# Performance work log

Measured on AMD Instinct MI355X. Metric: run time of the kernel, lower is better.

## Reference

```python
import jax, jax.numpy as jnp
import numpy as np

EPS = 1.1920929e-07  # torch RMSNorm default eps = finfo(float32).eps


def segsum(a):
    # a: (..., T) -> (..., T, T); [i, j] = sum_{j < t <= i} a[t] for j <= i, -inf above diag
    T = a.shape[-1]
    cs = jnp.cumsum(a, axis=-1)
    diff = cs[..., :, None] - cs[..., None, :]
    mask = jnp.tril(jnp.ones((T, T), dtype=bool))
    return jnp.where(mask, diff, -jnp.inf)


def dw_causal_conv(x, w):
    # x: (B, L, C), w: (C, K) depthwise causal conv (left pad K-1), matches Conv1d(pad=K-1)[:, :L]
    K = w.shape[-1]
    L = x.shape[1]
    xp = jnp.pad(x, ((0, 0), (K - 1, 0), (0, 0)))
    out = jnp.zeros_like(x)
    for j in range(K):
        out = out + xp[:, j:j + L, :] * w[:, j]
    return out


def ssd(X, A, Bv, Cv, block_len, init_state):
    # X: (B,L,H,P) pre-multiplied by dt; A: (B,L,H) = A*dt; Bv/Cv: (B,L,H,N)
    Bsz, L, H, P = X.shape
    N = Bv.shape[-1]
    c = L // block_len
    Xb = X.reshape(Bsz, c, block_len, H, P)
    Bb = Bv.reshape(Bsz, c, block_len, H, N)
    Cb = Cv.reshape(Bsz, c, block_len, H, N)
    Ab = A.reshape(Bsz, c, block_len, H).transpose(0, 3, 1, 2)  # (B,H,c,l)
    A_cumsum = jnp.cumsum(Ab, axis=-1)
    Ltri = jnp.exp(segsum(Ab))  # (B,H,c,l,l)
    # intra-chunk (diagonal block) output
    Y_diag = jnp.einsum('bclhn,bcshn,bhcls,bcshp->bclhp', Cb, Bb, Ltri, Xb)
    # per-chunk final states
    decay_states = jnp.exp(A_cumsum[..., -1:] - A_cumsum)  # (B,H,c,l)
    states = jnp.einsum('bclhn,bhcl,bclhp->bchpn', Bb, decay_states, Xb)
    states = jnp.concatenate([init_state[:, None], states], axis=1)  # (B,c+1,H,P,N)
    # inter-chunk recurrence via segsum over chunk boundaries
    last_A = A_cumsum[..., -1]  # (B,H,c)
    decay_chunk = jnp.exp(segsum(jnp.pad(last_A, ((0, 0), (0, 0), (1, 0)))))  # (B,H,c+1,c+1)
    new_states = jnp.einsum('bhzc,bchpn->bzhpn', decay_chunk, states)
    states, final_state = new_states[:, :-1], new_states[:, -1]
    # off-diagonal contribution from carried-in states
    state_decay_out = jnp.exp(A_cumsum)  # (B,H,c,l)
    Y_off = jnp.einsum('bclhn,bchpn,bhcl->bclhp', Cb, states, state_decay_out)
    Y = (Y_diag + Y_off).reshape(Bsz, L, H, P)
    return Y, final_state


def setup_inputs():
    key = jax.random.key(0)
    ks = jax.random.split(key, 8)
    d_model, d_state, d_conv, expand, headdim, ngroups = 1024, 128, 4, 2, 64, 1
    d_inner = expand * d_model                      # 2048
    H = d_inner // headdim                          # 32
    proj_out = 2 * d_inner + 2 * ngroups * d_state + H  # 4384
    conv_dim = d_inner + 2 * ngroups * d_state      # 2304
    B, L = 2, 2048
    x = jax.random.normal(ks[0], (B, L, d_model), dtype=jnp.float32)
    state = jnp.zeros((B, H, headdim, d_state), dtype=jnp.float32)
    in_proj_w = jax.random.normal(ks[1], (proj_out, d_model), dtype=jnp.float32) * 0.02
    conv_w = jax.random.normal(ks[2], (conv_dim, d_conv), dtype=jnp.float32) * 0.2
    A_log = jnp.log(jax.random.uniform(ks[3], (H,), minval=1.0, maxval=16.0))
    dt0 = jnp.exp(jax.random.uniform(ks[4], (H,)) * (np.log(0.1) - np.log(0.001)) + np.log(0.001))
    dt0 = jnp.maximum(dt0, 0.0001)
    dt_bias = dt0 + jnp.log(-jnp.expm1(-dt0))
    D_param = jnp.ones((H,), dtype=jnp.float32)
    norm_w = jnp.ones((d_inner,), dtype=jnp.float32)
    out_proj_w = jax.random.normal(ks[5], (d_model, d_inner), dtype=jnp.float32) * 0.02
    return dict(x=x, state=state, in_proj_w=in_proj_w, conv_w=conv_w, A_log=A_log,
                dt_bias=dt_bias, D_param=D_param, norm_w=norm_w, out_proj_w=out_proj_w,
                block_len=64)


def reference(x, state, in_proj_w, conv_w, A_log, dt_bias, D_param, norm_w, out_proj_w, block_len):
    B, L, Dm = x.shape
    H = A_log.shape[0]
    P = state.shape[2]
    N = state.shape[3]
    d_inner = H * P
    conv_dim = conv_w.shape[0]
    zxbcdt = x @ in_proj_w.T  # (B,L,proj_out)
    z = zxbcdt[..., :d_inner]
    xBC = zxbcdt[..., d_inner:d_inner + conv_dim]
    dt = zxbcdt[..., d_inner + conv_dim:]
    xBC = jax.nn.silu(dw_causal_conv(xBC, conv_w))
    x_branch = xBC[..., :d_inner]
    Bv = xBC[..., d_inner:d_inner + N]           # ngroups = 1
    Cv = xBC[..., d_inner + N:]
    X = jax.nn.silu(x_branch.reshape(B, L, H, P))
    Bv = jnp.broadcast_to(jax.nn.silu(Bv)[:, :, None, :], (B, L, H, N))
    Cv = jnp.broadcast_to(jax.nn.silu(Cv)[:, :, None, :], (B, L, H, N))
    A = -jnp.exp(A_log)
    dt = jax.nn.softplus(dt + dt_bias)           # (B,L,H)
    A_dt = A * dt
    X_dt = X * dt[..., None]
    Y, final_state = ssd(X_dt, A_dt, Bv, Cv, block_len, state)
    Y = Y + D_param[None, None, :, None] * X
    y_flat = Y.reshape(B, L, d_inner)
    y_norm = y_flat * jax.lax.rsqrt(jnp.mean(y_flat * y_flat, axis=-1, keepdims=True) + EPS) * norm_w
    y_core = y_norm * jax.nn.sigmoid(z)
    y = y_core @ out_proj_w.T + x
    return (y, final_state)
```

## Files before the change

kernel.cpp:

```cpp
#include <hip/hip_runtime.h>
#include <math.h>

#define BATCH 2
#define LSEQ  2048
#define TTOK  4096
#define DM    1024
#define DI    2048
#define NH    32
#define HP    64
#define NS    128
#define CONVD 2304
#define PROJ  4384
#define NCH   32
#define BLK   64

typedef __bf16 bf16x8 __attribute__((ext_vector_type(8)));
typedef float  f32x4  __attribute__((ext_vector_type(4)));
typedef unsigned short ushortx8 __attribute__((ext_vector_type(8)));
typedef unsigned short ushort_t;
typedef __attribute__((address_space(3))) void  lds_void;
typedef __attribute__((address_space(1))) const void glb_cvoid;

__device__ __forceinline__ float silu_(float x) { return x / (1.f + __expf(-x)); }

__device__ __forceinline__ unsigned short f2bf(float x) {
    union { float f; unsigned u; } u; u.f = x;
    unsigned r = u.u + 0x7fffu + ((u.u >> 16) & 1u);
    return (unsigned short)(r >> 16);
}
__device__ __forceinline__ float bf2f(unsigned short s) {
    union { unsigned u; float f; } u; u.u = ((unsigned)s) << 16; return u.f;
}

__global__ __launch_bounds__(256)
void cast_all_k(const float* __restrict__ x, const float* __restrict__ ipw,
                const float* __restrict__ opw,
                ushort_t* __restrict__ xb, ushort_t* __restrict__ ipb,
                ushort_t* __restrict__ opb)
{
    const int n1 = TTOK*DM, n2 = PROJ*DM;
    int i = (blockIdx.x * 256 + threadIdx.x) * 8;
    const float* src; ushort_t* dst;
    if (i < n1)            { src = x   + i;             dst = xb  + i; }
    else if (i < n1 + n2)  { src = ipw + (i - n1);      dst = ipb + (i - n1); }
    else                   { src = opw + (i - n1 - n2); dst = opb + (i - n1 - n2); }
    float4 a = *(const float4*)(src);
    float4 b = *(const float4*)(src + 4);
    ushortx8 r;
    r[0]=f2bf(a.x); r[1]=f2bf(a.y); r[2]=f2bf(a.z); r[3]=f2bf(a.w);
    r[4]=f2bf(b.x); r[5]=f2bf(b.y); r[6]=f2bf(b.z); r[7]=f2bf(b.w);
    *(ushortx8*)dst = r;
}

template<int HASRES, int OUTBF>
__global__ __launch_bounds__(256)
void hgemm_nt(const ushort_t* __restrict__ A, const ushort_t* __restrict__ Bw,
              void* __restrict__ Cp, const float* __restrict__ R,
              int M, int N, int K)
{
    __shared__ ushort_t As[128 * 32];
    __shared__ ushort_t Bs[128 * 32];
    const int t = threadIdx.x;
    const int l = t & 63, w = t >> 6;
    const int tx_ = (N + 127) >> 7, ty_ = (M + 127) >> 7;
    int bid = blockIdx.x;
    int sc = bid / (8 * ty_), rem = bid % (8 * ty_);
    int sw_w = min(8, tx_ - sc * 8);
    int bx = sc * 8 + rem % sw_w;
    int by = rem / sw_w;
    const int bm = by * 128, bn = bx * 128;
    const int wm = (w >> 1) * 64, wn = (w & 1) * 64;

    const int srow = t >> 2;
    const int skk  = (t & 3) * 8;
    const ushort_t* Ag0 = A + (size_t)(bm + srow)      * K + skk;
    const ushort_t* Ag1 = A + (size_t)(bm + 64 + srow) * K + skk;
    const int bn0 = min(bn + srow, N - 1), bn1 = min(bn + 64 + srow, N - 1);
    const ushort_t* Bg0 = Bw + (size_t)bn0 * K + skk;
    const ushort_t* Bg1 = Bw + (size_t)bn1 * K + skk;
    char* As0 = (char*)As;
    char* Bs0 = (char*)Bs;
    const int la0 = 16 * t;
    const int la1 = 4096 + 16 * t;

    f32x4 acc[4][4] = {};
    const int fr = l & 15, koff = (l >> 4) * 8;

    for (int k0 = 0; k0 < K; k0 += 32) {
        __syncthreads();
        __builtin_amdgcn_global_load_lds((glb_cvoid*)(Ag0 + k0), (lds_void*)(As0 + la0), 16, 0, 0);
        __builtin_amdgcn_global_load_lds((glb_cvoid*)(Ag1 + k0), (lds_void*)(As0 + la1), 16, 0, 0);
        __builtin_amdgcn_global_load_lds((glb_cvoid*)(Bg0 + k0), (lds_void*)(Bs0 + la0), 16, 0, 0);
        __builtin_amdgcn_global_load_lds((glb_cvoid*)(Bg1 + k0), (lds_void*)(Bs0 + la1), 16, 0, 0);
        __syncthreads();
        bf16x8 af[4], bfr[4];
#pragma unroll
        for (int mt = 0; mt < 4; ++mt)
            af[mt] = *(const bf16x8*)(As + (wm + mt * 16 + fr) * 32 + koff);
#pragma unroll
        for (int nt = 0; nt < 4; ++nt)
            bfr[nt] = *(const bf16x8*)(Bs + (wn + nt * 16 + fr) * 32 + koff);
#pragma unroll
        for (int mt = 0; mt < 4; ++mt)
#pragma unroll
            for (int nt = 0; nt < 4; ++nt)
                acc[mt][nt] = __builtin_amdgcn_mfma_f32_16x16x32_bf16(af[mt], bfr[nt], acc[mt][nt], 0, 0, 0);
    }

    const int crow = (l >> 4) * 4, ccol = l & 15;
#pragma unroll
    for (int mt = 0; mt < 4; ++mt) {
#pragma unroll
        for (int nt = 0; nt < 4; ++nt) {
            int n = bn + wn + nt * 16 + ccol;
            if (n >= N) continue;
#pragma unroll
            for (int i = 0; i < 4; ++i) {
                int m = bm + wm + mt * 16 + crow + i;
                float v = acc[mt][nt][i];
                if (HASRES) v += R[(size_t)m * N + n];
                if (OUTBF) ((ushort_t*)Cp)[(size_t)m * N + n] = f2bf(v);
                else       ((float*)Cp)[(size_t)m * N + n] = v;
            }
        }
    }
}

#define NCONVB 9216
__global__ __launch_bounds__(256)
void mid1_k(const ushort_t* __restrict__ zx, const float* __restrict__ cw,
            const float* __restrict__ dt_bias, const float* __restrict__ A_log,
            ushort_t* __restrict__ xBC, float* __restrict__ dt_sp, float* __restrict__ cumA)
{
    if (blockIdx.x < NCONVB) {
        int idx = blockIdx.x * 256 + threadIdx.x;
        int c4 = (idx % (CONVD/4)) * 4;
        int tkk = idx / (CONVD/4);
        int b = tkk >> 11, l = tkk & 2047;
        const ushort_t* col = zx + (size_t)b * LSEQ * PROJ + DI + c4;
        float4 w0 = *(const float4*)(cw + c4*4);
        float4 w1 = *(const float4*)(cw + c4*4 + 4);
        float4 w2 = *(const float4*)(cw + c4*4 + 8);
        float4 w3 = *(const float4*)(cw + c4*4 + 12);
        ushort4 tp = *(const ushort4*)(col + (size_t)l * PROJ);
        float a0 = w0.w * bf2f(tp.x), a1 = w1.w * bf2f(tp.y), a2 = w2.w * bf2f(tp.z), a3 = w3.w * bf2f(tp.w);
        if (l >= 1) { ushort4 v = *(const ushort4*)(col + (size_t)(l-1) * PROJ);
            a0 += w0.z*bf2f(v.x); a1 += w1.z*bf2f(v.y); a2 += w2.z*bf2f(v.z); a3 += w3.z*bf2f(v.w); }
        if (l >= 2) { ushort4 v = *(const ushort4*)(col + (size_t)(l-2) * PROJ);
            a0 += w0.y*bf2f(v.x); a1 += w1.y*bf2f(v.y); a2 += w2.y*bf2f(v.z); a3 += w3.y*bf2f(v.w); }
        if (l >= 3) { ushort4 v = *(const ushort4*)(col + (size_t)(l-3) * PROJ);
            a0 += w0.x*bf2f(v.x); a1 += w1.x*bf2f(v.y); a2 += w2.x*bf2f(v.z); a3 += w3.x*bf2f(v.w); }
        ushort4 o;
        o.x = f2bf(silu_(silu_(a0))); o.y = f2bf(silu_(silu_(a1)));
        o.z = f2bf(silu_(silu_(a2))); o.w = f2bf(silu_(silu_(a3)));
        *(ushort4*)(xBC + (size_t)tkk * CONVD + c4) = o;
    } else {
        int wid = (blockIdx.x - NCONVB) * 4 + (threadIdx.x >> 6);
        int ln = threadIdx.x & 63;
        int c = wid & 31, h = (wid >> 5) & 31, b = wid >> 10;
        int tk = b * LSEQ + c * BLK + ln;
        float xv = bf2f(zx[(size_t)tk * PROJ + (DI + CONVD) + h]) + dt_bias[h];
        float dtv = (xv > 20.f) ? xv : log1pf(__expf(xv));
        dt_sp[tk * NH + h] = dtv;
        float val = -__expf(A_log[h]) * dtv;
#pragma unroll
        for (int off = 1; off < 64; off <<= 1) {
            float u = __shfl_up(val, off, 64);
            if (ln >= off) val += u;
        }
        cumA[(size_t)wid * 64 + ln] = val;
    }
}

__global__ __launch_bounds__(256)
void mid2_k(const ushort_t* __restrict__ xBC, const float* __restrict__ dt_sp,
            const float* __restrict__ cumA, float* __restrict__ CBT,
            float* __restrict__ states)
{
    __shared__ __align__(16) char smem[33408];
    int t = threadIdx.x, r = t >> 2, q = t & 3;
    if (blockIdx.x < 64) {
        int b = blockIdx.x >> 5, c = blockIdx.x & 31;
        float (*sB)[65] = (float(*)[65])smem;
        float (*sC)[65] = sB + 64;
        const ushort_t* xb = xBC + (size_t)(b * LSEQ + c * BLK) * CONVD;
        float acc[16];
#pragma unroll
        for (int i = 0; i < 16; ++i) acc[i] = 0.f;
        for (int half = 0; half < 2; ++half) {
            __syncthreads();
#pragma unroll
            for (int jj = 0; jj < 4; ++jj) {
                ushort4 bv = *(const ushort4*)(xb + (size_t)r * CONVD + DI      + half*64 + q*16 + jj*4);
                ushort4 cv = *(const ushort4*)(xb + (size_t)r * CONVD + DI + NS + half*64 + q*16 + jj*4);
                int col = q*16 + jj*4;
                sB[r][col]=bf2f(bv.x); sB[r][col+1]=bf2f(bv.y); sB[r][col+2]=bf2f(bv.z); sB[r][col+3]=bf2f(bv.w);
                sC[r][col]=bf2f(cv.x); sC[r][col+1]=bf2f(cv.y); sC[r][col+2]=bf2f(cv.z); sC[r][col+3]=bf2f(cv.w);
            }
            __syncthreads();
            for (int n = 0; n < 64; ++n) {
                float cv = sC[r][n];
#pragma unroll
                for (int si = 0; si < 16; ++si)
                    acc[si] += cv * sB[q*16 + si][n];
            }
        }
        float* o = CBT + (size_t)blockIdx.x * 4096 + r * 64 + q * 16;
#pragma unroll
        for (int si = 0; si < 16; ++si) o[si] = acc[si];
    } else {
        int bi = blockIdx.x - 64;
        int h = bi & 31, c = (bi >> 5) & 31, b = bi >> 10;
        ushort_t* XdT = (ushort_t*)smem;
        ushort_t* BdT = XdT + 64 * 72;
        const float* cA = cumA + (size_t)((b*NH + h)*NCH + c) * 64;
        float scale = dt_sp[(b * LSEQ + c * BLK + r) * NH + h] * __expf(cA[63] - cA[r]);
        const ushort_t* xb = xBC + (size_t)(b * LSEQ + c * BLK + r) * CONVD;
#pragma unroll
        for (int jj = 0; jj < 4; ++jj) {
            ushort4 v = *(const ushort4*)(xb + h*HP + q*16 + jj*4);
            int p0 = q*16 + jj*4;
            XdT[(p0+0)*72 + r] = v.x; XdT[(p0+1)*72 + r] = v.y;
            XdT[(p0+2)*72 + r] = v.z; XdT[(p0+3)*72 + r] = v.w;
        }
#pragma unroll
        for (int jj = 0; jj < 8; ++jj) {
            ushort4 v = *(const ushort4*)(xb + DI + q*32 + jj*4);
            int n0 = q*32 + jj*4;
            BdT[(n0+0)*72 + r] = f2bf(bf2f(v.x)*scale);
            BdT[(n0+1)*72 + r] = f2bf(bf2f(v.y)*scale);
            BdT[(n0+2)*72 + r] = f2bf(bf2f(v.z)*scale);
            BdT[(n0+3)*72 + r] = f2bf(bf2f(v.w)*scale);
        }
        __syncthreads();
        int ln = t & 63, w = t >> 6;
        int wm = (w >> 1) * 32, wn = (w & 1) * 64;
        int fr = ln & 15;
        f32x4 acc[2][4] = {};
#pragma unroll
        for (int ks = 0; ks < 2; ++ks) {
            int koff = ks*32 + (ln >> 4) * 8;
            bf16x8 af[2], bv[4];
#pragma unroll
            for (int mt = 0; mt < 2; ++mt) af[mt] = *(const bf16x8*)&XdT[(wm + mt*16 + fr)*72 + koff];
#pragma unroll
            for (int nt = 0; nt < 4; ++nt) bv[nt] = *(const bf16x8*)&BdT[(wn + nt*16 + fr)*72 + koff];
#pragma unroll
            for (int mt = 0; mt < 2; ++mt)
#pragma unroll
                for (int nt = 0; nt < 4; ++nt)
                    acc[mt][nt] = __builtin_amdgcn_mfma_f32_16x16x32_bf16(af[mt], bv[nt], acc[mt][nt], 0, 0, 0);
        }
        float* o = states + (size_t)((b*NCH + c)*NH + h) * 8192;
        int crow = (ln >> 4) * 4, ccol = ln & 15;
#pragma unroll
        for (int mt = 0; mt < 2; ++mt)
#pragma unroll
            for (int nt = 0; nt < 4; ++nt)
#pragma unroll
                for (int i = 0; i < 4; ++i)
                    o[(wm + mt*16 + crow + i)*128 + wn + nt*16 + ccol] = acc[mt][nt][i];
    }
}

__global__ __launch_bounds__(256)
void scan_k(const float* __restrict__ init_state, const float* __restrict__ cumA,
            const float* __restrict__ states, ushort_t* __restrict__ pref,
            float* __restrict__ out_final)
{
    int idx = blockIdx.x * 256 + threadIdx.x;
    int h = (idx >> 13) & 31, b = idx >> 18;
    int pn = idx & 8191;
    float run = init_state[idx];
    const float* cAb = cumA + (size_t)(b*NH + h) * NCH * 64;
    for (int c = 0; c < NCH; ++c) {
        float la = cAb[c*64 + 63];
        size_t off = (size_t)((b*NCH + c)*NH + h) * 8192 + pn;
        float tmp = states[off];
        pref[off] = f2bf(run);
        run = expf(la) * run + tmp;
    }
    out_final[idx] = run;
}

__global__ __launch_bounds__(256)
void y_mfma_k(const ushort_t* __restrict__ xBC, const float* __restrict__ dt_sp,
              const float* __restrict__ cumA, const float* __restrict__ CBT,
              const ushort_t* __restrict__ pref, const float* __restrict__ D_param,
              float* __restrict__ Y)
{
    int bi = blockIdx.x;
    int h = bi & 31, c = (bi >> 5) & 31, b = bi >> 10;
    __shared__ ushort_t Wm[64 * 72];
    __shared__ ushort_t XT[64 * 72];
    __shared__ ushort_t Cd[64 * 136];
    __shared__ ushort_t Sp[64 * 136];
    __shared__ float sCA[64];
    __shared__ float sdt[64];
    int t = threadIdx.x, r = t >> 2, q = t & 3;
    const float* cA = cumA + (size_t)((b*NH + h)*NCH + c) * 64;
    if (t < 64) {
        sCA[t] = cA[t];
        sdt[t] = dt_sp[(b * LSEQ + c * BLK + t) * NH + h];
    }
    __syncthreads();
    size_t row = (size_t)(b * LSEQ + c * BLK + r);
    const ushort_t* xb = xBC + row * CONVD;
    float myA = sCA[r], eC = __expf(myA);
    const float* cbt = CBT + (size_t)(b*NCH + c) * 4096 + r * 64;
#pragma unroll
    for (int j = 0; j < 16; ++j) {
        int s = q*16 + j;
        float wv = (s <= r) ? cbt[s] * __expf(myA - sCA[s]) * sdt[s] : 0.f;
        Wm[r*72 + s] = f2bf(wv);
    }
#pragma unroll
    for (int jj = 0; jj < 4; ++jj) {
        ushort4 v = *(const ushort4*)(xb + h*HP + q*16 + jj*4);
        int p0 = q*16 + jj*4;
        XT[(p0+0)*72 + r] = v.x; XT[(p0+1)*72 + r] = v.y;
        XT[(p0+2)*72 + r] = v.z; XT[(p0+3)*72 + r] = v.w;
    }
#pragma unroll
    for (int jj = 0; jj < 8; ++jj) {
        ushort4 v = *(const ushort4*)(xb + DI + NS + q*32 + jj*4);
        int n0 = q*32 + jj*4;
        Cd[r*136 + n0+0] = f2bf(bf2f(v.x)*eC);
        Cd[r*136 + n0+1] = f2bf(bf2f(v.y)*eC);
        Cd[r*136 + n0+2] = f2bf(bf2f(v.z)*eC);
        Cd[r*136 + n0+3] = f2bf(bf2f(v.w)*eC);
    }
    const ushort_t* pr = pref + (size_t)((b*NCH + c)*NH + h) * 8192 + r * 128;
#pragma unroll
    for (int jj = 0; jj < 4; ++jj) {
        ushortx8 v = *(const ushortx8*)(pr + q*32 + jj*8);
        *(ushortx8*)&Sp[r*136 + q*32 + jj*8] = v;
    }
    __syncthreads();
    int ln = t & 63, w = t >> 6;
    int wm = (w >> 1) * 32, wn = (w & 1) * 32;
    int fr = ln & 15;
    f32x4 acc[2][2] = {};
#pragma unroll
    for (int ks = 0; ks < 2; ++ks) {
        int koff = ks*32 + (ln >> 4) * 8;
        bf16x8 af[2], bv[2];
#pragma unroll
        for (int mt = 0; mt < 2; ++mt) af[mt] = *(const bf16x8*)&Wm[(wm + mt*16 + fr)*72 + koff];
#pragma unroll
        for (int nt = 0; nt < 2; ++nt) bv[nt] = *(const bf16x8*)&XT[(wn + nt*16 + fr)*72 + koff];
#pragma unroll
        for (int mt = 0; mt < 2; ++mt)
#pragma unroll
            for (int nt = 0; nt < 2; ++nt)
                acc[mt][nt] = __builtin_amdgcn_mfma_f32_16x16x32_bf16(af[mt], bv[nt], acc[mt][nt], 0, 0, 0);
    }
#pragma unroll
    for (int ks = 0; ks < 4; ++ks) {
        int koff = ks*32 + (ln >> 4) * 8;
        bf16x8 af[2], bv[2];
#pragma unroll
        for (int mt = 0; mt < 2; ++mt) af[mt] = *(const bf16x8*)&Cd[(wm + mt*16 + fr)*136 + koff];
#pragma unroll
        for (int nt = 0; nt < 2; ++nt) bv[nt] = *(const bf16x8*)&Sp[(wn + nt*16 + fr)*136 + koff];
#pragma unroll
        for (int mt = 0; mt < 2; ++mt)
#pragma unroll
            for (int nt = 0; nt < 2; ++nt)
                acc[mt][nt] = __builtin_amdgcn_mfma_f32_16x16x32_bf16(af[mt], bv[nt], acc[mt][nt], 0, 0, 0);
    }
    float Dh = D_param[h];
    int crow = (ln >> 4) * 4, ccol = ln & 15;
#pragma unroll
    for (int mt = 0; mt < 2; ++mt)
#pragma unroll
        for (int nt = 0; nt < 2; ++nt)
#pragma unroll
            for (int i = 0; i < 4; ++i) {
                int li = wm + mt*16 + crow + i;
                int p  = wn + nt*16 + ccol;
                size_t rr = (size_t)(b*LSEQ + c*BLK + li);
                float xv = bf2f(xBC[rr * CONVD + h*HP + p]);
                Y[rr * DI + h*HP + p] = acc[mt][nt][i] + Dh * xv;
            }
}

__global__ __launch_bounds__(256)
void rms_gate_k(const ushort_t* __restrict__ zx, const float* __restrict__ norm_w,
                const float* __restrict__ Y, ushort_t* __restrict__ Yb)
{
    int tk = blockIdx.x, t = threadIdx.x;
    const float* rowp = Y + (size_t)tk * DI;
    float4 v0 = *(const float4*)(rowp + t*4);
    float4 v1 = *(const float4*)(rowp + 1024 + t*4);
    float ss = v0.x*v0.x + v0.y*v0.y + v0.z*v0.z + v0.w*v0.w
             + v1.x*v1.x + v1.y*v1.y + v1.z*v1.z + v1.w*v1.w;
#pragma unroll
    for (int off = 32; off > 0; off >>= 1) ss += __shfl_xor(ss, off, 64);
    __shared__ float sw[4];
    __shared__ float stot;
    if ((t & 63) == 0) sw[t >> 6] = ss;
    __syncthreads();
    if (t == 0) stot = rsqrtf((sw[0]+sw[1]+sw[2]+sw[3]) * (1.f/DI) + 1.1920929e-07f);
    __syncthreads();
    float scale = stot;
    const ushort_t* zr = zx + (size_t)tk * PROJ;
    ushort4 z0 = *(const ushort4*)(zr + t*4);
    ushort4 z1 = *(const ushort4*)(zr + 1024 + t*4);
    float4 w0 = *(const float4*)(norm_w + t*4);
    float4 w1 = *(const float4*)(norm_w + 1024 + t*4);
    ushort4 o0, o1;
    o0.x = f2bf(v0.x*scale*w0.x / (1.f+__expf(-bf2f(z0.x))));
    o0.y = f2bf(v0.y*scale*w0.y / (1.f+__expf(-bf2f(z0.y))));
    o0.z = f2bf(v0.z*scale*w0.z / (1.f+__expf(-bf2f(z0.z))));
    o0.w = f2bf(v0.w*scale*w0.w / (1.f+__expf(-bf2f(z0.w))));
    o1.x = f2bf(v1.x*scale*w1.x / (1.f+__expf(-bf2f(z1.x))));
    o1.y = f2bf(v1.y*scale*w1.y / (1.f+__expf(-bf2f(z1.y))));
    o1.z = f2bf(v1.z*scale*w1.z / (1.f+__expf(-bf2f(z1.z))));
    o1.w = f2bf(v1.w*scale*w1.w / (1.f+__expf(-bf2f(z1.w))));
    *(ushort4*)(Yb + (size_t)tk * DI + t*4) = o0;
    *(ushort4*)(Yb + (size_t)tk * DI + 1024 + t*4) = o1;
}

extern "C" void kernel_launch(void* const* d_in, const int* in_sizes, int n_in,
                              void* d_out, int out_size, void* d_ws, size_t ws_size,
                              hipStream_t stream)
{
    const float* x        = (const float*)d_in[0];
    const float* init_st  = (const float*)d_in[1];
    const float* in_proj  = (const float*)d_in[2];
    const float* conv_w   = (const float*)d_in[3];
    const float* A_log    = (const float*)d_in[4];
    const float* dt_bias  = (const float*)d_in[5];
    const float* D_param  = (const float*)d_in[6];
    const float* norm_w   = (const float*)d_in[7];
    const float* out_proj = (const float*)d_in[8];
    float* out = (float*)d_out;

    ushort_t* zx_bf  = (ushort_t*)d_ws;
    ushort_t* xBC_bf = zx_bf + (size_t)TTOK*PROJ;
    float* dt_sp  = (float*)(xBC_bf + (size_t)TTOK*CONVD);
    float* cumA   = dt_sp  + (size_t)TTOK*NH;
    float* CBTb   = cumA   + (size_t)TTOK*NH;
    float* states = CBTb   + 262144;
    ushort_t* pref = (ushort_t*)(states + 16777216);
    float* Y      = (float*)(pref + 16777216);
    ushort_t* opw_bf = (ushort_t*)(Y + (size_t)TTOK*DI);
    ushort_t* xb_bf  = (ushort_t*)Y;
    ushort_t* ipw_bf = xb_bf + (size_t)TTOK*DM;
    ushort_t* Yb_bf  = xBC_bf;

    const int nc = (TTOK*DM + PROJ*DM + DM*DI) / (256*8);
    cast_all_k<<<nc, 256, 0, stream>>>(x, in_proj, out_proj, xb_bf, ipw_bf, opw_bf);
    hgemm_nt<0,1><<<((PROJ+127)/128)*(TTOK/128), 256, 0, stream>>>(xb_bf, ipw_bf, zx_bf, nullptr, TTOK, PROJ, DM);
    mid1_k<<<NCONVB + BATCH*NH*NCH/4, 256, 0, stream>>>(zx_bf, conv_w, dt_bias, A_log, xBC_bf, dt_sp, cumA);
    mid2_k<<<64 + BATCH*NCH*NH, 256, 0, stream>>>(xBC_bf, dt_sp, cumA, CBTb, states);
    scan_k<<<(BATCH*NH*HP*NS)/256, 256, 0, stream>>>(init_st, cumA, states, pref, out + (size_t)TTOK*DM);
    y_mfma_k<<<BATCH*NCH*NH, 256, 0, stream>>>(xBC_bf, dt_sp, cumA, CBTb, pref, D_param, Y);
    rms_gate_k<<<TTOK, 256, 0, stream>>>(zx_bf, norm_w, Y, Yb_bf);
    hgemm_nt<1,0><<<(DM/128)*(TTOK/128), 256, 0, stream>>>(Yb_bf, opw_bf, out, x, TTOK, DM, DI);
}
```

Baseline: 329.5 us.

## Templatize GEMM tiles with K=64 steps, store Y in bf16, vectorize RMS gate

After: 338.4 us. 1.03x slower.

```diff
diff --git a/kernel.cpp b/kernel.cpp
--- a/kernel.cpp
+++ b/kernel.cpp
@@ -52,66 +52,78 @@
     *(ushortx8*)dst = r;
 }
 
-template<int HASRES, int OUTBF>
+template<int TM, int TN, int HASRES, int OUTBF>
 __global__ __launch_bounds__(256)
 void hgemm_nt(const ushort_t* __restrict__ A, const ushort_t* __restrict__ Bw,
               void* __restrict__ Cp, const float* __restrict__ R,
               int M, int N, int K)
 {
-    __shared__ ushort_t As[128 * 32];
-    __shared__ ushort_t Bs[128 * 32];
+    constexpr int JA = TM / 32, JB = TN / 32;
+    constexpr int MT = TM / 32, NT = TN / 32;
+    __shared__ ushort_t S[(TM + TN) * 64];
+    ushort_t* As = S;
+    ushort_t* Bs = S + TM * 64;
+    char* As_c = (char*)As;
+    char* Bs_c = (char*)Bs;
     const int t = threadIdx.x;
     const int l = t & 63, w = t >> 6;
-    const int tx_ = (N + 127) >> 7, ty_ = (M + 127) >> 7;
+
+    const int tx_ = (N + TN - 1) / TN, ty_ = (M + TM - 1) / TM;
     int bid = blockIdx.x;
     int sc = bid / (8 * ty_), rem = bid % (8 * ty_);
     int sw_w = min(8, tx_ - sc * 8);
     int bx = sc * 8 + rem % sw_w;
     int by = rem / sw_w;
-    const int bm = by * 128, bn = bx * 128;
-    const int wm = (w >> 1) * 64, wn = (w & 1) * 64;
-
-    const int srow = t >> 2;
-    const int skk  = (t & 3) * 8;
-    const ushort_t* Ag0 = A + (size_t)(bm + srow)      * K + skk;
-    const ushort_t* Ag1 = A + (size_t)(bm + 64 + srow) * K + skk;
-    const int bn0 = min(bn + srow, N - 1), bn1 = min(bn + 64 + srow, N - 1);
-    const ushort_t* Bg0 = Bw + (size_t)bn0 * K + skk;
-    const ushort_t* Bg1 = Bw + (size_t)bn1 * K + skk;
-    char* As0 = (char*)As;
-    char* Bs0 = (char*)Bs;
-    const int la0 = 16 * t;
-    const int la1 = 4096 + 16 * t;
-
-    f32x4 acc[4][4] = {};
-    const int fr = l & 15, koff = (l >> 4) * 8;
-
-    for (int k0 = 0; k0 < K; k0 += 32) {
+    const int bm = by * TM, bn = bx * TN;
+    const int wm = (w >> 1) * (TM / 2), wn = (w & 1) * (TN / 2);
+
+    const int rowt = t >> 3;
+    const int kkt  = (t & 7) * 8;
+    const ushort_t* srcA = A + (size_t)(bm + rowt) * K + kkt;
+    const ushort_t* srcB[JB];
+#pragma unroll
+    for (int j = 0; j < JB; ++j) {
+        int gr = min(bn + j * 32 + rowt, N - 1);
+        srcB[j] = Bw + (size_t)gr * K + kkt;
+    }
+
+    f32x4 acc[MT][NT] = {};
+    const int fr = l & 15, sel8 = (l >> 4) * 8;
+
+    for (int k0 = 0; k0 < K; k0 += 64) {
         __syncthreads();
-        __builtin_amdgcn_global_load_lds((glb_cvoid*)(Ag0 + k0), (lds_void*)(As0 + la0), 16, 0, 0);
-        __builtin_amdgcn_global_load_lds((glb_cvoid*)(Ag1 + k0), (lds_void*)(As0 + la1), 16, 0, 0);
-        __builtin_amdgcn_global_load_lds((glb_cvoid*)(Bg0 + k0), (lds_void*)(Bs0 + la0), 16, 0, 0);
-        __builtin_amdgcn_global_load_lds((glb_cvoid*)(Bg1 + k0), (lds_void*)(Bs0 + la1), 16, 0, 0);
+#pragma unroll
+        for (int j = 0; j < JA; ++j)
+            __builtin_amdgcn_global_load_lds((glb_cvoid*)(srcA + (size_t)j * 32 * K + k0),
+                                             (lds_void*)(As_c + 4096 * j + 16 * t), 16, 0, 0);
+#pragma unroll
+        for (int j = 0; j < JB; ++j)
+            __builtin_amdgcn_global_load_lds((glb_cvoid*)(srcB[j] + k0),
+                                             (lds_void*)(Bs_c + 4096 * j + 16 * t), 16, 0, 0);
         __syncthreads();
-        bf16x8 af[4], bfr[4];
-#pragma unroll
-        for (int mt = 0; mt < 4; ++mt)
-            af[mt] = *(const bf16x8*)(As + (wm + mt * 16 + fr) * 32 + koff);
-#pragma unroll
-        for (int nt = 0; nt < 4; ++nt)
-            bfr[nt] = *(const bf16x8*)(Bs + (wn + nt * 16 + fr) * 32 + koff);
-#pragma unroll
-        for (int mt = 0; mt < 4; ++mt)
-#pragma unroll
-            for (int nt = 0; nt < 4; ++nt)
-                acc[mt][nt] = __builtin_amdgcn_mfma_f32_16x16x32_bf16(af[mt], bfr[nt], acc[mt][nt], 0, 0, 0);
+#pragma unroll
+        for (int ks = 0; ks < 2; ++ks) {
+            const int koff = ks * 32 + sel8;
+            bf16x8 af[MT], bfr[NT];
+#pragma unroll
+            for (int mt = 0; mt < MT; ++mt)
+                af[mt] = *(const bf16x8*)(As + (wm + mt * 16 + fr) * 64 + koff);
+#pragma unroll
+            for (int nt = 0; nt < NT; ++nt)
+                bfr[nt] = *(const bf16x8*)(Bs + (wn + nt * 16 + fr) * 64 + koff);
+#pragma unroll
+            for (int mt = 0; mt < MT; ++mt)
+#pragma unroll
+                for (int nt = 0; nt < NT; ++nt)
+                    acc[mt][nt] = __builtin_amdgcn_mfma_f32_16x16x32_bf16(af[mt], bfr[nt], acc[mt][nt], 0, 0, 0);
+        }
     }
 
     const int crow = (l >> 4) * 4, ccol = l & 15;
 #pragma unroll
-    for (int mt = 0; mt < 4; ++mt) {
-#pragma unroll
-        for (int nt = 0; nt < 4; ++nt) {
+    for (int mt = 0; mt < MT; ++mt) {
+#pragma unroll
+        for (int nt = 0; nt < NT; ++nt) {
             int n = bn + wn + nt * 16 + ccol;
             if (n >= N) continue;
 #pragma unroll
@@ -287,7 +299,7 @@
 void y_mfma_k(const ushort_t* __restrict__ xBC, const float* __restrict__ dt_sp,
               const float* __restrict__ cumA, const float* __restrict__ CBT,
               const ushort_t* __restrict__ pref, const float* __restrict__ D_param,
-              float* __restrict__ Y)
+              ushort_t* __restrict__ Y)
 {
     int bi = blockIdx.x;
     int h = bi & 31, c = (bi >> 5) & 31, b = bi >> 10;
@@ -381,20 +393,21 @@
                 int p  = wn + nt*16 + ccol;
                 size_t rr = (size_t)(b*LSEQ + c*BLK + li);
                 float xv = bf2f(xBC[rr * CONVD + h*HP + p]);
-                Y[rr * DI + h*HP + p] = acc[mt][nt][i] + Dh * xv;
+                Y[rr * DI + h*HP + p] = f2bf(acc[mt][nt][i] + Dh * xv);
             }
 }
 
 __global__ __launch_bounds__(256)
 void rms_gate_k(const ushort_t* __restrict__ zx, const float* __restrict__ norm_w,
-                const float* __restrict__ Y, ushort_t* __restrict__ Yb)
+                const ushort_t* __restrict__ Y, ushort_t* __restrict__ Yb)
 {
     int tk = blockIdx.x, t = threadIdx.x;
-    const float* rowp = Y + (size_t)tk * DI;
-    float4 v0 = *(const float4*)(rowp + t*4);
-    float4 v1 = *(const float4*)(rowp + 1024 + t*4);
-    float ss = v0.x*v0.x + v0.y*v0.y + v0.z*v0.z + v0.w*v0.w
-             + v1.x*v1.x + v1.y*v1.y + v1.z*v1.z + v1.w*v1.w;
+    const ushort_t* rowp = Y + (size_t)tk * DI + t*8;
+    ushortx8 v = *(const ushortx8*)rowp;
+    float f[8];
+    float ss = 0.f;
+#pragma unroll
+    for (int i = 0; i < 8; ++i) { f[i] = bf2f(v[i]); ss += f[i]*f[i]; }
 #pragma unroll
     for (int off = 32; off > 0; off >>= 1) ss += __shfl_xor(ss, off, 64);
     __shared__ float sw[4];
@@ -404,22 +417,16 @@
     if (t == 0) stot = rsqrtf((sw[0]+sw[1]+sw[2]+sw[3]) * (1.f/DI) + 1.1920929e-07f);
     __syncthreads();
     float scale = stot;
-    const ushort_t* zr = zx + (size_t)tk * PROJ;
-    ushort4 z0 = *(const ushort4*)(zr + t*4);
-    ushort4 z1 = *(const ushort4*)(zr + 1024 + t*4);
-    float4 w0 = *(const float4*)(norm_w + t*4);
-    float4 w1 = *(const float4*)(norm_w + 1024 + t*4);
-    ushort4 o0, o1;
-    o0.x = f2bf(v0.x*scale*w0.x / (1.f+__expf(-bf2f(z0.x))));
-    o0.y = f2bf(v0.y*scale*w0.y / (1.f+__expf(-bf2f(z0.y))));
-    o0.z = f2bf(v0.z*scale*w0.z / (1.f+__expf(-bf2f(z0.z))));
-    o0.w = f2bf(v0.w*scale*w0.w / (1.f+__expf(-bf2f(z0.w))));
-    o1.x = f2bf(v1.x*scale*w1.x / (1.f+__expf(-bf2f(z1.x))));
-    o1.y = f2bf(v1.y*scale*w1.y / (1.f+__expf(-bf2f(z1.y))));
-    o1.z = f2bf(v1.z*scale*w1.z / (1.f+__expf(-bf2f(z1.z))));
-    o1.w = f2bf(v1.w*scale*w1.w / (1.f+__expf(-bf2f(z1.w))));
-    *(ushort4*)(Yb + (size_t)tk * DI + t*4) = o0;
-    *(ushort4*)(Yb + (size_t)tk * DI + 1024 + t*4) = o1;
+    const ushort_t* zr = zx + (size_t)tk * PROJ + t*8;
+    ushortx8 z = *(const ushortx8*)zr;
+    float4 w0 = *(const float4*)(norm_w + t*8);
+    float4 w1 = *(const float4*)(norm_w + t*8 + 4);
+    float wv[8] = {w0.x,w0.y,w0.z,w0.w,w1.x,w1.y,w1.z,w1.w};
+    ushortx8 o;
+#pragma unroll
+    for (int i = 0; i < 8; ++i)
+        o[i] = f2bf(f[i]*scale*wv[i] / (1.f+__expf(-bf2f(z[i]))));
+    *(ushortx8*)(Yb + (size_t)tk * DI + t*8) = o;
 }
 
 extern "C" void kernel_launch(void* const* d_in, const int* in_sizes, int n_in,
@@ -444,19 +451,20 @@
     float* CBTb   = cumA   + (size_t)TTOK*NH;
     float* states = CBTb   + 262144;
     ushort_t* pref = (ushort_t*)(states + 16777216);
-    float* Y      = (float*)(pref + 16777216);
-    ushort_t* opw_bf = (ushort_t*)(Y + (size_t)TTOK*DI);
-    ushort_t* xb_bf  = (ushort_t*)Y;
+    float* Yreg   = (float*)(pref + 16777216);
+    ushort_t* opw_bf = (ushort_t*)(Yreg + (size_t)TTOK*DI);
+    ushort_t* Y_bf   = (ushort_t*)Yreg;
+    ushort_t* xb_bf  = (ushort_t*)Yreg;
     ushort_t* ipw_bf = xb_bf + (size_t)TTOK*DM;
     ushort_t* Yb_bf  = xBC_bf;
 
     const int nc = (TTOK*DM + PROJ*DM + DM*DI) / (256*8);
     cast_all_k<<<nc, 256, 0, stream>>>(x, in_proj, out_proj, xb_bf, ipw_bf, opw_bf);
-    hgemm_nt<0,1><<<((PROJ+127)/128)*(TTOK/128), 256, 0, stream>>>(xb_bf, ipw_bf, zx_bf, nullptr, TTOK, PROJ, DM);
+    hgemm_nt<128,128,0,1><<<((PROJ+127)/128)*(TTOK/128), 256, 0, stream>>>(xb_bf, ipw_bf, zx_bf, nullptr, TTOK, PROJ, DM);
     mid1_k<<<NCONVB + BATCH*NH*NCH/4, 256, 0, stream>>>(zx_bf, conv_w, dt_bias, A_log, xBC_bf, dt_sp, cumA);
     mid2_k<<<64 + BATCH*NCH*NH, 256, 0, stream>>>(xBC_bf, dt_sp, cumA, CBTb, states);
     scan_k<<<(BATCH*NH*HP*NS)/256, 256, 0, stream>>>(init_st, cumA, states, pref, out + (size_t)TTOK*DM);
-    y_mfma_k<<<BATCH*NCH*NH, 256, 0, stream>>>(xBC_bf, dt_sp, cumA, CBTb, pref, D_param, Y);
-    rms_gate_k<<<TTOK, 256, 0, stream>>>(zx_bf, norm_w, Y, Yb_bf);
-    hgemm_nt<1,0><<<(DM/128)*(TTOK/128), 256, 0, stream>>>(Yb_bf, opw_bf, out, x, TTOK, DM, DI);
-}
+    y_mfma_k<<<BATCH*NCH*NH, 256, 0, stream>>>(xBC_bf, dt_sp, cumA, CBTb, pref, D_param, Y_bf);
+    rms_gate_k<<<TTOK, 256, 0, stream>>>(zx_bf, norm_w, Y_bf, Yb_bf);
+    hgemm_nt<128,64,1,0><<<(DM/64)*(TTOK/128), 256, 0, stream>>>(Yb_bf, opw_bf, out, x, TTOK, DM, DI);
+}
```
